# Performance work log

Measured on AMD Instinct MI355X. Metric: run time of the kernel, lower is better.

Reference implementation:

```python
import jax, jax.numpy as jnp
import numpy as np

N = 4096  # rows == cols so the original's range(len(d1)) loop covers the full tensor
EPS = 1e-05


def setup_inputs() -> dict:
    key = jax.random.key(0)
    k1, k2 = jax.random.split(key)
    distribution1 = jax.random.uniform(k1, (N, N), dtype=jnp.float32)
    distribution2 = jax.random.uniform(k2, (N, N), dtype=jnp.float32)
    return {"distribution1": distribution1, "distribution2": distribution2}


def reference(distribution1, distribution2):
    d1 = jnp.squeeze(distribution1).astype(jnp.float32)
    d2 = jnp.squeeze(distribution2).astype(jnp.float32)
    # loss = sum_i [ -sum_j d1[i,j] * log(d2[i,j] + eps) ]  (fused elementwise + full reduce)
    loss = -jnp.sum(d1 * jnp.log(d2 + EPS))
    return loss.reshape(1)
```

## Files before the change

### kernel.cpp

```cpp
#include <hip/hip_runtime.h>
#include <math.h>


#define EPS 1e-5f
#define BLOCK 256
#define PAIRS 2
#define STAGES 4

__global__ __launch_bounds__(BLOCK) void cep_loss_kernel(
        const float4* __restrict__ d1,
        const float4* __restrict__ d2,
        float* __restrict__ partials,
        int n4) {
    int tid = blockIdx.x * blockDim.x + threadIdx.x;
    int stride = gridDim.x * blockDim.x;

    float acc0 = 0.0f, acc1 = 0.0f, acc2 = 0.0f, acc3 = 0.0f;

    float4 a0[PAIRS], b0[PAIRS], a1[PAIRS], b1[PAIRS];

    int base = tid;
    #pragma unroll
    for (int p = 0; p < PAIRS; p++) {
        a0[p] = d1[base + p * stride];
        b0[p] = d2[base + p * stride];
    }

    #pragma unroll
    for (int s = 1; s < STAGES; s++) {
        int nb = base + PAIRS * stride;
        #pragma unroll
        for (int p = 0; p < PAIRS; p++) {
            a1[p] = d1[nb + p * stride];
            b1[p] = d2[nb + p * stride];
        }
        #pragma unroll
        for (int p = 0; p < PAIRS; p++) {
            acc0 += a0[p].x * __logf(b0[p].x + EPS);
            acc1 += a0[p].y * __logf(b0[p].y + EPS);
            acc2 += a0[p].z * __logf(b0[p].z + EPS);
            acc3 += a0[p].w * __logf(b0[p].w + EPS);
        }
        #pragma unroll
        for (int p = 0; p < PAIRS; p++) { a0[p] = a1[p]; b0[p] = b1[p]; }
        base = nb;
    }

    #pragma unroll
    for (int p = 0; p < PAIRS; p++) {
        acc0 += a0[p].x * __logf(b0[p].x + EPS);
        acc1 += a0[p].y * __logf(b0[p].y + EPS);
        acc2 += a0[p].z * __logf(b0[p].z + EPS);
        acc3 += a0[p].w * __logf(b0[p].w + EPS);
    }

    float acc = (acc0 + acc1) + (acc2 + acc3);

    #pragma unroll
    for (int off = 32; off > 0; off >>= 1)
        acc += __shfl_down(acc, off, 64);

    __shared__ float wave_sums[BLOCK / 64];
    int lane = threadIdx.x & 63;
    int wid  = threadIdx.x >> 6;
    if (lane == 0) wave_sums[wid] = acc;
    __syncthreads();

    if (threadIdx.x == 0) {
        float s = wave_sums[0] + wave_sums[1] + wave_sums[2] + wave_sums[3];
        partials[blockIdx.x] = s;
    }
}

__global__ __launch_bounds__(BLOCK) void cep_final_kernel(
        const float* __restrict__ partials, float* __restrict__ out, int nparts) {
    float acc = 0.0f;
    for (int i = threadIdx.x; i < nparts; i += BLOCK)
        acc += partials[i];

    #pragma unroll
    for (int off = 32; off > 0; off >>= 1)
        acc += __shfl_down(acc, off, 64);

    __shared__ float wave_sums[BLOCK / 64];
    int lane = threadIdx.x & 63;
    int wid  = threadIdx.x >> 6;
    if (lane == 0) wave_sums[wid] = acc;
    __syncthreads();

    if (threadIdx.x == 0) {
        float s = wave_sums[0] + wave_sums[1] + wave_sums[2] + wave_sums[3];
        out[0] = -s;
    }
}

extern "C" void kernel_launch(void* const* d_in, const int* in_sizes, int n_in,
                              void* d_out, int out_size, void* d_ws, size_t ws_size,
                              hipStream_t stream) {
    const float4* d1 = (const float4*)d_in[0];
    const float4* d2 = (const float4*)d_in[1];
    float* out = (float*)d_out;
    float* partials = (float*)d_ws;

    int n = in_sizes[0];
    int n4 = n / 4;

    const int per_thread = STAGES * PAIRS;
    const int grid = n4 / (BLOCK * per_thread);

    cep_loss_kernel<<<grid, BLOCK, 0, stream>>>(d1, d2, partials, n4);
    cep_final_kernel<<<1, BLOCK, 0, stream>>>(partials, out, grid);
}
```

Before: 145.4 us.

## Fuse final reduction into main kernel via last-block atomic counter

Replaces the two-kernel reduction with a single kernel in which the last block to finish, found through an agent-scope atomic counter, sums the per-block partials. Loads are restructured into chunks of four float4 per input, separated from compute by a scheduling barrier, and the grid is fixed at 2048 blocks with launch bounds requesting higher occupancy. The aim is to remove the second kernel launch and improve memory-level parallelism. It adds a memset launch for the counter and hardcodes the problem size through GRID.

```diff
diff --git a/kernel.cpp b/kernel.cpp
--- a/kernel.cpp
+++ b/kernel.cpp
@@ -4,94 +4,115 @@
 
 #define EPS 1e-5f
 #define BLOCK 256
-#define PAIRS 2
-#define STAGES 4
+#define GRID 2048
+#define CHUNK 4
+#define CHUNKS 2
+
+__device__ __forceinline__ float block_reduce(float acc, float* wsum) {
+    #pragma unroll
+    for (int off = 32; off > 0; off >>= 1)
+        acc += __shfl_down(acc, off, 64);
+    int lane = threadIdx.x & 63;
+    int wid  = threadIdx.x >> 6;
+    if (lane == 0) wsum[wid] = acc;
+    __syncthreads();
+    return wsum[0] + wsum[1] + wsum[2] + wsum[3];
+}
+
+__global__ __launch_bounds__(BLOCK, 8) void cep_fused_kernel(
+        const float4* __restrict__ d1,
+        const float4* __restrict__ d2,
+        float* __restrict__ out,
+        float* __restrict__ partials,
+        unsigned int* __restrict__ counter) {
+    const int tid    = blockIdx.x * BLOCK + threadIdx.x;
+    const int stride = GRID * BLOCK;
+
+    float acc0 = 0.0f, acc1 = 0.0f, acc2 = 0.0f, acc3 = 0.0f;
+
+    int idx = tid;
+    #pragma unroll
+    for (int c = 0; c < CHUNKS; ++c) {
+        float4 y[CHUNK], x[CHUNK];
+        #pragma unroll
+        for (int p = 0; p < CHUNK; ++p) y[p] = d2[idx + p * stride];
+        #pragma unroll
+        for (int p = 0; p < CHUNK; ++p) x[p] = d1[idx + p * stride];
+        __builtin_amdgcn_sched_barrier(0);
+        #pragma unroll
+        for (int p = 0; p < CHUNK; ++p) {
+            acc0 = fmaf(x[p].x, __logf(y[p].x + EPS), acc0);
+            acc1 = fmaf(x[p].y, __logf(y[p].y + EPS), acc1);
+            acc2 = fmaf(x[p].z, __logf(y[p].z + EPS), acc2);
+            acc3 = fmaf(x[p].w, __logf(y[p].w + EPS), acc3);
+        }
+        idx += CHUNK * stride;
+    }
+
+    float acc = (acc0 + acc1) + (acc2 + acc3);
+
+    __shared__ float wsum[BLOCK / 64];
+    float bsum = block_reduce(acc, wsum);
+
+    __shared__ bool amlast;
+    if (threadIdx.x == 0) {
+        partials[blockIdx.x] = bsum;
+        unsigned prev = __hip_atomic_fetch_add(counter, 1u,
+                __ATOMIC_ACQ_REL, __HIP_MEMORY_SCOPE_AGENT);
+        amlast = (prev == GRID - 1);
+    }
+    __syncthreads();
+    if (!amlast) return;
+
+    float facc = 0.0f;
+    for (int i = threadIdx.x; i < GRID; i += BLOCK)
+        facc += __hip_atomic_load(&partials[i],
+                __ATOMIC_RELAXED, __HIP_MEMORY_SCOPE_AGENT);
+    __syncthreads();
+    float fsum = block_reduce(facc, wsum);
+    if (threadIdx.x == 0) out[0] = -fsum;
+}
+
 
 __global__ __launch_bounds__(BLOCK) void cep_loss_kernel(
         const float4* __restrict__ d1,
         const float4* __restrict__ d2,
-        float* __restrict__ partials,
-        int n4) {
-    int tid = blockIdx.x * blockDim.x + threadIdx.x;
-    int stride = gridDim.x * blockDim.x;
-
+        float* __restrict__ partials) {
+    const int tid    = blockIdx.x * BLOCK + threadIdx.x;
+    const int stride = GRID * BLOCK;
     float acc0 = 0.0f, acc1 = 0.0f, acc2 = 0.0f, acc3 = 0.0f;
-
-    float4 a0[PAIRS], b0[PAIRS], a1[PAIRS], b1[PAIRS];
-
-    int base = tid;
+    int idx = tid;
     #pragma unroll
-    for (int p = 0; p < PAIRS; p++) {
-        a0[p] = d1[base + p * stride];
-        b0[p] = d2[base + p * stride];
+    for (int c = 0; c < CHUNKS; ++c) {
+        float4 y[CHUNK], x[CHUNK];
+        #pragma unroll
+        for (int p = 0; p < CHUNK; ++p) y[p] = d2[idx + p * stride];
+        #pragma unroll
+        for (int p = 0; p < CHUNK; ++p) x[p] = d1[idx + p * stride];
+        __builtin_amdgcn_sched_barrier(0);
+        #pragma unroll
+        for (int p = 0; p < CHUNK; ++p) {
+            acc0 = fmaf(x[p].x, __logf(y[p].x + EPS), acc0);
+            acc1 = fmaf(x[p].y, __logf(y[p].y + EPS), acc1);
+            acc2 = fmaf(x[p].z, __logf(y[p].z + EPS), acc2);
+            acc3 = fmaf(x[p].w, __logf(y[p].w + EPS), acc3);
+        }
+        idx += CHUNK * stride;
     }
-
-    #pragma unroll
-    for (int s = 1; s < STAGES; s++) {
-        int nb = base + PAIRS * stride;
-        #pragma unroll
-        for (int p = 0; p < PAIRS; p++) {
-            a1[p] = d1[nb + p * stride];
-            b1[p] = d2[nb + p * stride];
-        }
-        #pragma unroll
-        for (int p = 0; p < PAIRS; p++) {
-            acc0 += a0[p].x * __logf(b0[p].x + EPS);
-            acc1 += a0[p].y * __logf(b0[p].y + EPS);
-            acc2 += a0[p].z * __logf(b0[p].z + EPS);
-            acc3 += a0[p].w * __logf(b0[p].w + EPS);
-        }
-        #pragma unroll
-        for (int p = 0; p < PAIRS; p++) { a0[p] = a1[p]; b0[p] = b1[p]; }
-        base = nb;
-    }
-
-    #pragma unroll
-    for (int p = 0; p < PAIRS; p++) {
-        acc0 += a0[p].x * __logf(b0[p].x + EPS);
-        acc1 += a0[p].y * __logf(b0[p].y + EPS);
-        acc2 += a0[p].z * __logf(b0[p].z + EPS);
-        acc3 += a0[p].w * __logf(b0[p].w + EPS);
-    }
-
     float acc = (acc0 + acc1) + (acc2 + acc3);
-
-    #pragma unroll
-    for (int off = 32; off > 0; off >>= 1)
-        acc += __shfl_down(acc, off, 64);
-
-    __shared__ float wave_sums[BLOCK / 64];
-    int lane = threadIdx.x & 63;
-    int wid  = threadIdx.x >> 6;
-    if (lane == 0) wave_sums[wid] = acc;
-    __syncthreads();
-
-    if (threadIdx.x == 0) {
-        float s = wave_sums[0] + wave_sums[1] + wave_sums[2] + wave_sums[3];
-        partials[blockIdx.x] = s;
-    }
+    __shared__ float wsum[BLOCK / 64];
+    float bsum = block_reduce(acc, wsum);
+    if (threadIdx.x == 0) partials[blockIdx.x] = bsum;
 }
 
 __global__ __launch_bounds__(BLOCK) void cep_final_kernel(
-        const float* __restrict__ partials, float* __restrict__ out, int nparts) {
+        const float* __restrict__ partials, float* __restrict__ out) {
     float acc = 0.0f;
-    for (int i = threadIdx.x; i < nparts; i += BLOCK)
+    for (int i = threadIdx.x; i < GRID; i += BLOCK)
         acc += partials[i];
-
-    #pragma unroll
-    for (int off = 32; off > 0; off >>= 1)
-        acc += __shfl_down(acc, off, 64);
-
-    __shared__ float wave_sums[BLOCK / 64];
-    int lane = threadIdx.x & 63;
-    int wid  = threadIdx.x >> 6;
-    if (lane == 0) wave_sums[wid] = acc;
-    __syncthreads();
-
-    if (threadIdx.x == 0) {
-        float s = wave_sums[0] + wave_sums[1] + wave_sums[2] + wave_sums[3];
-        out[0] = -s;
-    }
+    __shared__ float wsum[BLOCK / 64];
+    float fsum = block_reduce(acc, wsum);
+    if (threadIdx.x == 0) out[0] = -fsum;
 }
 
 extern "C" void kernel_launch(void* const* d_in, const int* in_sizes, int n_in,
@@ -99,15 +120,16 @@
                               hipStream_t stream) {
     const float4* d1 = (const float4*)d_in[0];
     const float4* d2 = (const float4*)d_in[1];
-    float* out = (float*)d_out;
+    float* out      = (float*)d_out;
     float* partials = (float*)d_ws;
 
-    int n = in_sizes[0];
-    int n4 = n / 4;
-
-    const int per_thread = STAGES * PAIRS;
-    const int grid = n4 / (BLOCK * per_thread);
-
-    cep_loss_kernel<<<grid, BLOCK, 0, stream>>>(d1, d2, partials, n4);
-    cep_final_kernel<<<1, BLOCK, 0, stream>>>(partials, out, grid);
+    const size_t need = (size_t)GRID * sizeof(float) + sizeof(unsigned int);
+    if (ws_size >= need) {
+        unsigned int* counter = (unsigned int*)((char*)d_ws + GRID * sizeof(float));
+        hipMemsetAsync(counter, 0, sizeof(unsigned int), stream);
+        cep_fused_kernel<<<GRID, BLOCK, 0, stream>>>(d1, d2, out, partials, counter);
+    } else {
+        cep_loss_kernel<<<GRID, BLOCK, 0, stream>>>(d1, d2, partials);
+        cep_final_kernel<<<1, BLOCK, 0, stream>>>(partials, out);
+    }
 }
```

After: 245.6 us. 68.9% more time.

## Deepen load pipeline with inline-asm loads and explicit vmcnt waits

Applied to the files above, without the earlier changes.

Replaces the two-deep compiler-scheduled prefetch with hand-written global_load_dwordx4 inline assembly that keeps four load pairs in flight, paced by explicit s_waitcnt vmcnt counts and sched barriers. Grid size and stride are hardcoded to 2048 blocks, which matches the old computed grid for N=4096. The goal is more memory-level parallelism per thread for this bandwidth-bound reduction. The cost is fragility: the kernel now assumes the fixed input size and depends on the vmcnt accounting matching the exact order in which loads are issued.

```diff
diff --git a/kernel.cpp b/kernel.cpp
--- a/kernel.cpp
+++ b/kernel.cpp
@@ -4,55 +4,59 @@
 
 #define EPS 1e-5f
 #define BLOCK 256
-#define PAIRS 2
-#define STAGES 4
+#define GRID 2048
+#define STRIDE (GRID * BLOCK)
+
+typedef float f4v __attribute__((ext_vector_type(4)));
+
+#define LOAD2(Y, X, PB, PA)                                   \
+    asm volatile("global_load_dwordx4 %0, %2, off\n\t"        \
+                 "global_load_dwordx4 %1, %3, off"            \
+                 : "=&v"(Y), "=&v"(X)                         \
+                 : "v"(PB), "v"(PA)                           \
+                 : "memory")
+
+#define WAITV(N)                                              \
+    do {                                                      \
+        asm volatile("s_waitcnt vmcnt(" #N ")" ::: "memory"); \
+        __builtin_amdgcn_sched_barrier(0);                    \
+    } while (0)
+
+#define CP(X, Y)                                              \
+    do {                                                      \
+        acc0 = fmaf((X).x, __logf((Y).x + EPS), acc0);        \
+        acc1 = fmaf((X).y, __logf((Y).y + EPS), acc1);        \
+        acc2 = fmaf((X).z, __logf((Y).z + EPS), acc2);        \
+        acc3 = fmaf((X).w, __logf((Y).w + EPS), acc3);        \
+    } while (0)
 
 __global__ __launch_bounds__(BLOCK) void cep_loss_kernel(
-        const float4* __restrict__ d1,
-        const float4* __restrict__ d2,
-        float* __restrict__ partials,
-        int n4) {
-    int tid = blockIdx.x * blockDim.x + threadIdx.x;
-    int stride = gridDim.x * blockDim.x;
+        const f4v* __restrict__ d1,
+        const f4v* __restrict__ d2,
+        float* __restrict__ partials) {
+    const int tid = blockIdx.x * BLOCK + threadIdx.x;
+    const f4v* pa = d1 + tid;
+    const f4v* pb = d2 + tid;
 
     float acc0 = 0.0f, acc1 = 0.0f, acc2 = 0.0f, acc3 = 0.0f;
 
-    float4 a0[PAIRS], b0[PAIRS], a1[PAIRS], b1[PAIRS];
+    f4v x0, x1, x2, x3, x4, x5, x6, x7;
+    f4v y0, y1, y2, y3, y4, y5, y6, y7;
 
-    int base = tid;
-    #pragma unroll
-    for (int p = 0; p < PAIRS; p++) {
-        a0[p] = d1[base + p * stride];
-        b0[p] = d2[base + p * stride];
-    }
+    LOAD2(y0, x0, pb, pa); pb += STRIDE; pa += STRIDE;
+    LOAD2(y1, x1, pb, pa); pb += STRIDE; pa += STRIDE;
+    LOAD2(y2, x2, pb, pa); pb += STRIDE; pa += STRIDE;
+    LOAD2(y3, x3, pb, pa); pb += STRIDE; pa += STRIDE;
 
-    #pragma unroll
-    for (int s = 1; s < STAGES; s++) {
-        int nb = base + PAIRS * stride;
-        #pragma unroll
-        for (int p = 0; p < PAIRS; p++) {
-            a1[p] = d1[nb + p * stride];
-            b1[p] = d2[nb + p * stride];
-        }
-        #pragma unroll
-        for (int p = 0; p < PAIRS; p++) {
-            acc0 += a0[p].x * __logf(b0[p].x + EPS);
-            acc1 += a0[p].y * __logf(b0[p].y + EPS);
-            acc2 += a0[p].z * __logf(b0[p].z + EPS);
-            acc3 += a0[p].w * __logf(b0[p].w + EPS);
-        }
-        #pragma unroll
-        for (int p = 0; p < PAIRS; p++) { a0[p] = a1[p]; b0[p] = b1[p]; }
-        base = nb;
-    }
+    WAITV(6); LOAD2(y4, x4, pb, pa); pb += STRIDE; pa += STRIDE; CP(x0, y0);
+    WAITV(6); LOAD2(y5, x5, pb, pa); pb += STRIDE; pa += STRIDE; CP(x1, y1);
+    WAITV(6); LOAD2(y6, x6, pb, pa); pb += STRIDE; pa += STRIDE; CP(x2, y2);
+    WAITV(6); LOAD2(y7, x7, pb, pa);                             CP(x3, y3);
 
-    #pragma unroll
-    for (int p = 0; p < PAIRS; p++) {
-        acc0 += a0[p].x * __logf(b0[p].x + EPS);
-        acc1 += a0[p].y * __logf(b0[p].y + EPS);
-        acc2 += a0[p].z * __logf(b0[p].z + EPS);
-        acc3 += a0[p].w * __logf(b0[p].w + EPS);
-    }
+    WAITV(6); CP(x4, y4);
+    WAITV(4); CP(x5, y5);
+    WAITV(2); CP(x6, y6);
+    WAITV(0); CP(x7, y7);
 
     float acc = (acc0 + acc1) + (acc2 + acc3);
 
@@ -97,17 +101,11 @@
 extern "C" void kernel_launch(void* const* d_in, const int* in_sizes, int n_in,
                               void* d_out, int out_size, void* d_ws, size_t ws_size,
                               hipStream_t stream) {
-    const float4* d1 = (const float4*)d_in[0];
-    const float4* d2 = (const float4*)d_in[1];
-    float* out = (float*)d_out;
+    const f4v* d1 = (const f4v*)d_in[0];
+    const f4v* d2 = (const f4v*)d_in[1];
+    float* out      = (float*)d_out;
     float* partials = (float*)d_ws;
 
-    int n = in_sizes[0];
-    int n4 = n / 4;
-
-    const int per_thread = STAGES * PAIRS;
-    const int grid = n4 / (BLOCK * per_thread);
-
-    cep_loss_kernel<<<grid, BLOCK, 0, stream>>>(d1, d2, partials, n4);
-    cep_final_kernel<<<1, BLOCK, 0, stream>>>(partials, out, grid);
+    cep_loss_kernel<<<GRID, BLOCK, 0, stream>>>(d1, d2, partials);
+    cep_final_kernel<<<1, BLOCK, 0, stream>>>(partials, out, GRID);
 }
```

Result: no change. 147.1 us (+1.2%).
